# Kernel optimization log

Measured on AMD Instinct MI355X. Metric: run time of the kernel, lower is better.

Reference implementation:

```python
import jax, jax.numpy as jnp
import numpy as np

# ---- static config (mirrors DRR.__init__ kwargs) ----
NX = NY = NZ = 192            # volume dims
H = W = 192                   # detector height/width
SDR = 300.0                   # source-to-rotation-center distance
DELX = DELY = 2.0             # detector pixel pitch (mm)
X0 = Y0 = 0.0                 # detector offsets
SPACING = (1.0, 1.0, 1.0)     # voxel spacing (mm)
BAM = 1.0                     # bone_attenuation_multiplier
B = 2                         # batch (poses)
N_SUB = H * W // 2            # p_subsample = 0.5


def setup_inputs() -> dict:
    key = jax.random.key(0)
    k1, k2, k3, k4 = jax.random.split(key, 4)
    # CT volume in Hounsfield units, spanning air (-1000) to bone (~2000)
    volume = jax.random.uniform(k1, (NX, NY, NZ), jnp.float32, -1000.0, 2000.0)
    rotations = jax.random.normal(k2, (B, 3), jnp.float32)          # Euler ZYX (rad)
    translations = jax.random.normal(k3, (B, 3), jnp.float32) * 10.0  # mm, near isocenter
    # unique subsampled detector pixel indices (Detector.subsamples[-1])
    subsample_idx = jax.random.permutation(k4, H * W)[:N_SUB].astype(jnp.int32)
    return {"volume": volume, "rotations": rotations,
            "translations": translations, "subsample_idx": subsample_idx}


def _rz(t):
    c, s = jnp.cos(t), jnp.sin(t); z = jnp.zeros_like(t); o = jnp.ones_like(t)
    return jnp.stack([jnp.stack([c, -s, z], -1),
                      jnp.stack([s, c, z], -1),
                      jnp.stack([z, z, o], -1)], -2)


def _ry(t):
    c, s = jnp.cos(t), jnp.sin(t); z = jnp.zeros_like(t); o = jnp.ones_like(t)
    return jnp.stack([jnp.stack([c, z, s], -1),
                      jnp.stack([z, o, z], -1),
                      jnp.stack([-s, z, c], -1)], -2)


def _rx(t):
    c, s = jnp.cos(t), jnp.sin(t); z = jnp.zeros_like(t); o = jnp.ones_like(t)
    return jnp.stack([jnp.stack([o, z, z], -1),
                      jnp.stack([z, c, -s], -1),
                      jnp.stack([z, s, c], -1)], -2)


def _density(volume):
    # DRR.__init__: volume.flip([0]); air/soft/bone HU segmentation + normalization
    vol = jnp.flip(volume, 0)
    soft = (vol > -800.0) & (vol <= 350.0)
    soft_min = jnp.min(jnp.where(soft, vol, jnp.inf))
    d = jnp.where(vol <= -800.0, soft_min,
                  jnp.where(vol > 350.0, vol * BAM, vol))
    d = d - jnp.min(d)
    return d / jnp.max(d)


def _canonical_detector():
    # source on +z at SDR, detector plane at -z; pixel grid with pitch delx/dely
    xs = (jnp.arange(W, dtype=jnp.float32) - (W - 1) / 2.0) * DELX + X0
    ys = (jnp.arange(H, dtype=jnp.float32) - (H - 1) / 2.0) * DELY + Y0
    gy, gx = jnp.meshgrid(ys, xs, indexing="ij")
    tgt = jnp.stack([gx.ravel(), gy.ravel(),
                     jnp.full((H * W,), -SDR, jnp.float32)], -1)  # [H*W, 3]
    src = jnp.array([0.0, 0.0, SDR], jnp.float32)
    return src, tgt


def _siddon(density, source, target):
    """Siddon ray-casting. source [B,3], target [B,N,3] -> line integrals [B,N]."""
    dims = density.shape
    sp = jnp.asarray(SPACING, density.dtype)
    src = source[:, None, :]                     # [B,1,3]
    sdd = target - src                           # [B,N,3]
    sdd_safe = jnp.where(sdd == 0, 1e-9, sdd)
    # parametric intersections with all grid planes per axis
    alist = [(jnp.arange(dims[a] + 1, dtype=density.dtype)[None, None, :] * sp[a]
              - src[..., a:a + 1]) / sdd_safe[..., a:a + 1] for a in range(3)]
    a_first = jnp.stack([al[..., 0] for al in alist], -1)    # [B,N,3]
    a_last = jnp.stack([al[..., -1] for al in alist], -1)
    amin = jnp.maximum(jnp.max(jnp.minimum(a_first, a_last), -1), 0.0)[..., None]
    amax = jnp.minimum(jnp.min(jnp.maximum(a_first, a_last), -1), 1.0)[..., None]
    amax = jnp.maximum(amax, amin)               # ray misses -> zero-length segments
    alphas = jnp.sort(jnp.clip(jnp.concatenate(alist, -1), amin, amax), -1)  # [B,N,M+1]
    mid = 0.5 * (alphas[..., 1:] + alphas[..., :-1])                         # [B,N,M]
    ray_len = jnp.linalg.norm(target - src, axis=-1, keepdims=True)
    step = (alphas[..., 1:] - alphas[..., :-1]) * ray_len                    # [B,N,M]
    pts = src[..., None, :] + mid[..., None] * sdd[..., None, :]             # [B,N,M,3]
    idx = jnp.clip(jnp.floor(pts / sp).astype(jnp.int32), 0,
                   jnp.array(dims, jnp.int32) - 1)
    vox = density[idx[..., 0], idx[..., 1], idx[..., 2]]                     # gather
    return jnp.sum(step * vox, -1)


def reference(volume, rotations, translations, subsample_idx):
    density = _density(volume)
    src_c, tgt_c = _canonical_detector()
    tgt_c = tgt_c[subsample_idx]                                  # [N,3] subsampled rays
    R = _rz(rotations[:, 0]) @ _ry(rotations[:, 1]) @ _rx(rotations[:, 2])  # [B,3,3]
    center = jnp.array([NX, NY, NZ], jnp.float32) * jnp.asarray(SPACING, jnp.float32) / 2.0
    t = translations + center                                     # pose about isocenter
    source = jnp.einsum("bij,j->bi", R, src_c) + t                # [B,3]
    target = jnp.einsum("bij,nj->bni", R, tgt_c) + t[:, None, :]  # [B,N,3]
    img = _siddon(density, source, target)                        # [B,N]
    # reshape_subsampled_drr: scatter into zeros [B, H*W] then view [B,1,H,W]
    drr = jnp.zeros((img.shape[0], H * W), img.dtype).at[:, subsample_idx].set(img)
    return drr.reshape(-1, 1, H, W)
```

## Files before the change

### kernel.cpp

```cpp
#include <hip/hip_runtime.h>
#include <float.h>
#include <math.h>


#define NDIM   192
#define HW     (NDIM * NDIM)
#define NSUB   (HW / 2)
#define NTILE  576
#define NBATCH 2
#define NCHUNK 16
#define NVOX   (NDIM * NDIM * NDIM)
#define SDRF   300.0f
#define RBLK   1728

#define WS_LIST_OFF 16
#define WS_PART_OFF (WS_LIST_OFF + 4 * NSUB)

__global__ __launch_bounds__(256) void reduce_kernel(
    const float* __restrict__ vol, float* __restrict__ parts) {
    const int tid = blockIdx.x * 256 + threadIdx.x;
    const float4* __restrict__ v4 = (const float4*)vol;
    const int S = RBLK * 256;

    float4 r0 = v4[tid + 0 * S];
    float4 r1 = v4[tid + 1 * S];
    float4 r2 = v4[tid + 2 * S];
    float4 r3 = v4[tid + 3 * S];

    float smin = FLT_MAX, rmin = FLT_MAX, rmax = -FLT_MAX;
    float4 rr[4] = {r0, r1, r2, r3};
#pragma unroll
    for (int k = 0; k < 4; ++k) {
        float xs[4] = {rr[k].x, rr[k].y, rr[k].z, rr[k].w};
#pragma unroll
        for (int j = 0; j < 4; ++j) {
            float x = xs[j];
            bool in = (x > -800.0f);
            rmin = fminf(rmin, in ? x : FLT_MAX);
            rmax = fmaxf(rmax, in ? x : -FLT_MAX);
            smin = fminf(smin, (in && x <= 350.0f) ? x : FLT_MAX);
        }
    }
#pragma unroll
    for (int off = 32; off > 0; off >>= 1) {
        smin = fminf(smin, __shfl_down(smin, off));
        rmin = fminf(rmin, __shfl_down(rmin, off));
        rmax = fmaxf(rmax, __shfl_down(rmax, off));
    }
    __shared__ float sm[4], rm[4], rx[4];
    int w = threadIdx.x >> 6;
    if ((threadIdx.x & 63) == 0) { sm[w] = smin; rm[w] = rmin; rx[w] = rmax; }
    __syncthreads();
    if (threadIdx.x == 0) {
        parts[blockIdx.x] =
            fminf(fminf(sm[0], sm[1]), fminf(sm[2], sm[3]));
        parts[RBLK + blockIdx.x] =
            fminf(fminf(rm[0], rm[1]), fminf(rm[2], rm[3]));
        parts[2 * RBLK + blockIdx.x] =
            fmaxf(fmaxf(rx[0], rx[1]), fmaxf(rx[2], rx[3]));
    }
}

__global__ __launch_bounds__(1024) void prep_kernel(
    const float* __restrict__ parts, const int* __restrict__ sidx,
    float* __restrict__ ws, int* __restrict__ list) {
    __shared__ unsigned int bits[HW / 32];
    __shared__ int cnts[NTILE];
    __shared__ float red0[16], red1[16], red2[16];

    const int tid = threadIdx.x;

    float smin = FLT_MAX, rmin = FLT_MAX, rmax = -FLT_MAX;
    for (int i = tid; i < RBLK; i += 1024) {
        smin = fminf(smin, parts[i]);
        rmin = fminf(rmin, parts[RBLK + i]);
        rmax = fmaxf(rmax, parts[2 * RBLK + i]);
    }
#pragma unroll
    for (int off = 32; off > 0; off >>= 1) {
        smin = fminf(smin, __shfl_down(smin, off));
        rmin = fminf(rmin, __shfl_down(rmin, off));
        rmax = fmaxf(rmax, __shfl_down(rmax, off));
    }
    int w = tid >> 6;
    if ((tid & 63) == 0) { red0[w] = smin; red1[w] = rmin; red2[w] = rmax; }

    for (int i = tid; i < HW / 32; i += 1024) bits[i] = 0u;
    __syncthreads();
    if (tid == 0) {
        float a = FLT_MAX, b = FLT_MAX, c = -FLT_MAX;
#pragma unroll
        for (int k = 0; k < 16; ++k) {
            a = fminf(a, red0[k]);
            b = fminf(b, red1[k]);
            c = fmaxf(c, red2[k]);
        }
        ws[0] = a; ws[1] = b; ws[2] = c;
    }

    for (int i = tid; i < NSUB; i += 1024) {
        int p = sidx[i];
        atomicOr(&bits[p >> 5], 1u << (p & 31));
    }
    __syncthreads();

    const unsigned char* bb = (const unsigned char*)bits;
    int myc = 0;
    int ti = tid / 24, tj = tid % 24;
    if (tid < NTILE) {
#pragma unroll
        for (int r = 0; r < 8; ++r)
            myc += __popc((int)bb[(ti * 8 + r) * 24 + tj]);
        cnts[tid] = myc;
    }
    __syncthreads();

    for (int off = 1; off < NTILE; off <<= 1) {
        int v = 0, u = 0;
        if (tid < NTILE) {
            v = cnts[tid];
            if (tid >= off) u = cnts[tid - off];
        }
        __syncthreads();
        if (tid < NTILE) cnts[tid] = v + u;
        __syncthreads();
    }

    if (tid < NTILE) {
        int o = cnts[tid] - myc;
#pragma unroll
        for (int r = 0; r < 8; ++r) {
            int pibase = (ti * 8 + r) * NDIM + tj * 8;
            unsigned int m = (unsigned int)bb[(ti * 8 + r) * 24 + tj];
            while (m) {
                int j = __ffs(m) - 1;
                m &= m - 1u;
                list[o++] = pibase + j;
            }
        }
    }
}

__device__ __forceinline__ void init_axis(float s, float d, float a_lo,
                                          int& i, int& st, float& na) {
    if (d > 0.0f) {
        st = 1;
        float f = s + a_lo * d;
        int ii = (int)floorf(f) + 1;
        ii = max(0, min(ii, NDIM + 1));
        while (ii <= NDIM && ((float)ii - s) / d <= a_lo) ++ii;
        while (ii > 0 && ((float)(ii - 1) - s) / d > a_lo) --ii;
        i  = ii;
        na = (ii <= NDIM) ? ((float)ii - s) / d : FLT_MAX;
    } else {
        st = -1;
        float f = s + a_lo * d;
        int ii = (int)ceilf(f) - 1;
        ii = max(-1, min(ii, NDIM));
        while (ii >= 0 && ((float)ii - s) / d <= a_lo) --ii;
        while (ii < NDIM && ((float)(ii + 1) - s) / d > a_lo) ++ii;
        i  = ii;
        na = (ii >= 0) ? ((float)ii - s) / d : FLT_MAX;
    }
}

__global__ __launch_bounds__(256) void ray_kernel(
    const float* __restrict__ vol, const float* __restrict__ rot,
    const float* __restrict__ trans, const float* __restrict__ wsc,
    const int* __restrict__ list, float* __restrict__ out) {
    const int n = blockIdx.x * 256 + threadIdx.x;
    const int c = blockIdx.y;
    const int b = blockIdx.z;

    const int p  = list[n];
    const int pi = p / NDIM;
    const int pj = p % NDIM;

    float smin = wsc[0];
    float rmin = wsc[1];
    float rmax = wsc[2];
    float dmin = fminf(smin, rmin);
    float dmax = fmaxf(smin, rmax);
    float scale = 1.0f / (dmax - dmin);

    float rz = rot[b * 3 + 0], ry = rot[b * 3 + 1], rx = rot[b * 3 + 2];
    float cz = cosf(rz), sz = sinf(rz);
    float cy = cosf(ry), sy = sinf(ry);
    float cx = cosf(rx), sx = sinf(rx);
    float R00 = cz * cy;
    float R01 = cz * sy * sx - sz * cx;
    float R02 = sz * sx + cz * sy * cx;
    float R10 = sz * cy;
    float R11 = cz * cx + sz * sy * sx;
    float R12 = sz * sy * cx - cz * sx;
    float R20 = -sy;
    float R21 = cy * sx;
    float R22 = cy * cx;
    float tx = trans[b * 3 + 0] + 96.0f;
    float ty = trans[b * 3 + 1] + 96.0f;
    float tz = trans[b * 3 + 2] + 96.0f;

    float srcx = R02 * SDRF + tx;
    float srcy = R12 * SDRF + ty;
    float srcz = R22 * SDRF + tz;
    float gx = ((float)pj - 95.5f) * 2.0f;
    float gy = ((float)pi - 95.5f) * 2.0f;
    float tgx = R00 * gx + R01 * gy + R02 * (-SDRF) + tx;
    float tgy = R10 * gx + R11 * gy + R12 * (-SDRF) + ty;
    float tgz = R20 * gx + R21 * gy + R22 * (-SDRF) + tz;

    float sdx = tgx - srcx, sdy = tgy - srcy, sdz = tgz - srcz;
    float dsx = (sdx == 0.0f) ? 1e-9f : sdx;
    float dsy = (sdy == 0.0f) ? 1e-9f : sdy;
    float dsz = (sdz == 0.0f) ? 1e-9f : sdz;

    float af0 = (0.0f - srcx) / dsx, al0 = (192.0f - srcx) / dsx;
    float af1 = (0.0f - srcy) / dsy, al1 = (192.0f - srcy) / dsy;
    float af2 = (0.0f - srcz) / dsz, al2 = (192.0f - srcz) / dsz;
    float amin = fmaxf(fmaxf(fminf(af0, al0), fminf(af1, al1)), fminf(af2, al2));
    amin = fmaxf(amin, 0.0f);
    float amax = fminf(fminf(fmaxf(af0, al0), fmaxf(af1, al1)), fmaxf(af2, al2));
    amax = fminf(amax, 1.0f);
    amax = fmaxf(amax, amin);
    float ray_len = sqrtf(sdx * sdx + sdy * sdy + sdz * sdz);

    float span = amax - amin;
    float a_lo = amin + span * ((float)c / (float)NCHUNK);
    float a_hi = (c == NCHUNK - 1) ? amax
                                   : amin + span * ((float)(c + 1) / (float)NCHUNK);

    int i0, i1, i2, st0, st1, st2;
    float na0, na1, na2;
    init_axis(srcx, dsx, a_lo, i0, st0, na0);
    init_axis(srcy, dsy, a_lo, i1, st1, na1);
    init_axis(srcz, dsz, a_lo, i2, st2, na2);

    float r0 = 1.0f / dsx, r1 = 1.0f / dsy, r2 = 1.0f / dsz;
    float fi0 = (float)i0, fi1 = (float)i1, fi2 = (float)i2;
    float fs0 = (float)st0, fs1 = (float)st1, fs2 = (float)st2;

    float cur = a_lo;
    float acc = 0.0f;
    while (true) {
        float an  = fminf(fminf(na0, na1), na2);
        bool fin  = !(an < a_hi);
        float a2  = fin ? a_hi : an;
        float mid = 0.5f * (cur + a2);
        float px = fmaf(mid, sdx, srcx);
        float py = fmaf(mid, sdy, srcy);
        float pz = fmaf(mid, sdz, srcz);
        int ix = min(max((int)px, 0), NDIM - 1);
        int iy = min(max((int)py, 0), NDIM - 1);
        int iz = min(max((int)pz, 0), NDIM - 1);
        int addr = (NDIM - 1) * HW - ix * HW + iy * NDIM + iz;
        float v  = vol[addr];
        float dv = (v <= -800.0f) ? smin : v;
        acc = fmaf(a2 - cur, dv, acc);
        if (fin) break;
        cur = a2;
        bool c0 = (na0 == an), c1 = (na1 == an), c2 = (na2 == an);
        float nf0 = fi0 + fs0, nf1 = fi1 + fs1, nf2 = fi2 + fs2;
        float nn0 = (nf0 - srcx) * r0;
        float nn1 = (nf1 - srcy) * r1;
        float nn2 = (nf2 - srcz) * r2;
        fi0 = c0 ? nf0 : fi0;  na0 = c0 ? nn0 : na0;
        fi1 = c1 ? nf1 : fi1;  na1 = c1 ? nn1 : na1;
        fi2 = c2 ? nf2 : fi2;  na2 = c2 ? nn2 : na2;
    }
    float res = (acc - dmin * (a_hi - a_lo)) * scale * ray_len;
    atomicAdd(&out[b * HW + p], res);
}

extern "C" void kernel_launch(void* const* d_in, const int* in_sizes, int n_in,
                              void* d_out, int out_size, void* d_ws,
                              size_t ws_size, hipStream_t stream) {
    const float* vol   = (const float*)d_in[0];
    const float* rot   = (const float*)d_in[1];
    const float* trans = (const float*)d_in[2];
    const int*   sidx  = (const int*)d_in[3];
    float* out = (float*)d_out;

    float* wsf   = (float*)d_ws;
    int*   list  = (int*)((unsigned char*)d_ws + WS_LIST_OFF);
    float* parts = (float*)((unsigned char*)d_ws + WS_PART_OFF);

    hipMemsetAsync(d_out, 0, (size_t)out_size * sizeof(float), stream);

    reduce_kernel<<<RBLK, 256, 0, stream>>>(vol, parts);
    prep_kernel<<<1, 1024, 0, stream>>>(parts, sidx, wsf, list);
    dim3 rgrid(NSUB / 256, NCHUNK, NBATCH);
    ray_kernel<<<rgrid, 256, 0, stream>>>(vol, rot, trans, wsf, list, out);
}
```

Before: 132.2 us.

## Software-pipeline Siddon ray march with precomputed step count and four in-flight loads

After: 125.7 us. 1.05x faster.

```diff
diff --git a/kernel.cpp b/kernel.cpp
--- a/kernel.cpp
+++ b/kernel.cpp
@@ -12,6 +12,7 @@
 #define NVOX   (NDIM * NDIM * NDIM)
 #define SDRF   300.0f
 #define RBLK   1728
+#define NBLKX  (NSUB / 256)
 
 #define WS_LIST_OFF 16
 #define WS_PART_OFF (WS_LIST_OFF + 4 * NSUB)
@@ -168,10 +169,10 @@
     const float* __restrict__ vol, const float* __restrict__ rot,
     const float* __restrict__ trans, const float* __restrict__ wsc,
     const int* __restrict__ list, float* __restrict__ out) {
-    const int n = blockIdx.x * 256 + threadIdx.x;
     const int c = blockIdx.y;
     const int b = blockIdx.z;
 
+    const int n = blockIdx.x * 256 + threadIdx.x;
     const int p  = list[n];
     const int pi = p / NDIM;
     const int pj = p % NDIM;
@@ -239,25 +240,27 @@
     float fi0 = (float)i0, fi1 = (float)i1, fi2 = (float)i2;
     float fs0 = (float)st0, fs1 = (float)st1, fs2 = (float)st2;
 
+    int T = 1;
+    if (na0 < a_hi) T += (int)((a_hi - na0) * fabsf(dsx)) + 2;
+    if (na1 < a_hi) T += (int)((a_hi - na1) * fabsf(dsy)) + 2;
+    if (na2 < a_hi) T += (int)((a_hi - na2) * fabsf(dsz)) + 2;
+
     float cur = a_lo;
     float acc = 0.0f;
-    while (true) {
-        float an  = fminf(fminf(na0, na1), na2);
-        bool fin  = !(an < a_hi);
-        float a2  = fin ? a_hi : an;
-        float mid = 0.5f * (cur + a2);
+
+    auto ADV = [&](float& wseg, int& addr) {
+        float an = fminf(fminf(na0, na1), na2);
+        float ae = fminf(an, a_hi);
+        wseg = ae - cur;
+        float mid = 0.5f * (cur + ae);
         float px = fmaf(mid, sdx, srcx);
         float py = fmaf(mid, sdy, srcy);
         float pz = fmaf(mid, sdz, srcz);
         int ix = min(max((int)px, 0), NDIM - 1);
         int iy = min(max((int)py, 0), NDIM - 1);
         int iz = min(max((int)pz, 0), NDIM - 1);
-        int addr = (NDIM - 1) * HW - ix * HW + iy * NDIM + iz;
-        float v  = vol[addr];
-        float dv = (v <= -800.0f) ? smin : v;
-        acc = fmaf(a2 - cur, dv, acc);
-        if (fin) break;
-        cur = a2;
+        addr = (NDIM - 1) * HW - ix * HW + iy * NDIM + iz;
+        cur = ae;
         bool c0 = (na0 == an), c1 = (na1 == an), c2 = (na2 == an);
         float nf0 = fi0 + fs0, nf1 = fi1 + fs1, nf2 = fi2 + fs2;
         float nn0 = (nf0 - srcx) * r0;
@@ -266,7 +269,30 @@
         fi0 = c0 ? nf0 : fi0;  na0 = c0 ? nn0 : na0;
         fi1 = c1 ? nf1 : fi1;  na1 = c1 ? nn1 : na1;
         fi2 = c2 ? nf2 : fi2;  na2 = c2 ? nn2 : na2;
-    }
+    };
+
+    float w0s, w1s, w2s, w3s;
+    int   ad0, ad1, ad2, ad3;
+    float v0, v1, v2, v3;
+    ADV(w0s, ad0); v0 = vol[ad0];
+    ADV(w1s, ad1); v1 = vol[ad1];
+    ADV(w2s, ad2); v2 = vol[ad2];
+    ADV(w3s, ad3); v3 = vol[ad3];
+    for (int s = 0; s < T; s += 4) {
+        float dv0 = (v0 <= -800.0f) ? smin : v0;
+        acc = fmaf(w0s, dv0, acc);
+        ADV(w0s, ad0); v0 = vol[ad0];
+        float dv1 = (v1 <= -800.0f) ? smin : v1;
+        acc = fmaf(w1s, dv1, acc);
+        ADV(w1s, ad1); v1 = vol[ad1];
+        float dv2 = (v2 <= -800.0f) ? smin : v2;
+        acc = fmaf(w2s, dv2, acc);
+        ADV(w2s, ad2); v2 = vol[ad2];
+        float dv3 = (v3 <= -800.0f) ? smin : v3;
+        acc = fmaf(w3s, dv3, acc);
+        ADV(w3s, ad3); v3 = vol[ad3];
+    }
+
     float res = (acc - dmin * (a_hi - a_lo)) * scale * ray_len;
     atomicAdd(&out[b * HW + p], res);
 }
@@ -288,6 +314,6 @@
 
     reduce_kernel<<<RBLK, 256, 0, stream>>>(vol, parts);
     prep_kernel<<<1, 1024, 0, stream>>>(parts, sidx, wsf, list);
-    dim3 rgrid(NSUB / 256, NCHUNK, NBATCH);
+    dim3 rgrid(NBLKX, NCHUNK, NBATCH);
     ray_kernel<<<rgrid, 256, 0, stream>>>(vol, rot, trans, wsf, list, out);
 }
```
